# Optimization experiments

Hardware: AMD Instinct MI355X
Metric: run time of the kernel (lower is better)

Reference implementation:

```python
import jax, jax.numpy as jnp
import numpy as np

N_NODES = 100000
N_EDGES = 1600000
IN_CH = 128
OUT_CH = 128
EDGE_DIM = 6
STATE_DIM = 5


def setup_inputs() -> dict:
    key = jax.random.key(0)
    k = jax.random.split(key, 8)
    x = jax.random.normal(k[0], (N_NODES, IN_CH), dtype=jnp.float32)
    edge_index = jax.random.randint(k[1], (2, N_EDGES), 0, N_NODES, dtype=jnp.int64)
    edge_attr = jax.random.normal(k[2], (N_EDGES, EDGE_DIM), dtype=jnp.float32)
    global_state = jax.random.normal(k[3], (N_NODES, STATE_DIM), dtype=jnp.float32)
    # learned params (glorot init for weights, zero bias like torch default-ish)
    d_neg_in = IN_CH + EDGE_DIM + STATE_DIM
    d_root_in = IN_CH + STATE_DIM
    s_neg = jnp.sqrt(6.0 / (d_neg_in + OUT_CH))
    s_root = jnp.sqrt(6.0 / (d_root_in + OUT_CH))
    W_neg = jax.random.uniform(k[4], (d_neg_in, OUT_CH), jnp.float32, -s_neg, s_neg)
    b_neg = jax.random.uniform(k[5], (OUT_CH,), jnp.float32, -0.05, 0.05)
    W_root = jax.random.uniform(k[6], (d_root_in, OUT_CH), jnp.float32, -s_root, s_root)
    b_root = jax.random.uniform(k[7], (OUT_CH,), jnp.float32, -0.05, 0.05)
    return {"x": x, "edge_index": edge_index, "edge_attr": edge_attr,
            "global_state": global_state, "W_neg": W_neg, "b_neg": b_neg,
            "W_root": W_root, "b_root": b_root}


def reference(x, edge_index, edge_attr, global_state, W_neg, b_neg, W_root, b_root):
    # x: [N, C], global_state: [N, S]
    xs = jnp.concatenate([x, global_state], axis=1)            # [N, C+S]
    src = xs[edge_index[1]]                                    # gather: [E, C+S]
    x_adj = jnp.concatenate([src, edge_attr], axis=1)          # [E, C+S+Ed]
    x_adj = jax.nn.elu(x_adj @ W_neg + b_neg)                  # [E, O]
    neg_sum = jax.ops.segment_sum(x_adj, edge_index[0], num_segments=xs.shape[0])  # [N, O]
    x_out = jax.nn.elu(xs @ W_root + b_root) + neg_sum         # [N, O]
    return x_out
```

## Files before the change

kernel.cpp:

```cpp
#include <hip/hip_runtime.h>
#include <hip/hip_bf16.h>
#include <math.h>

#define N_NODES 100000
#define N_EDGES 1600000
#define IN_CH 128
#define OUT_CH 128
#define EDGE_DIM 6
#define STATE_DIM 5
#define XS_DIM 133
#define KPAD 160
#define NKSTEP 5
#define ASTRIDE 168
#define NBLK 391
#define N_CHUNKS 25000

typedef short s16x8 __attribute__((ext_vector_type(8)));
typedef float f32x4 __attribute__((ext_vector_type(4)));
typedef _Float16 h16x2 __attribute__((ext_vector_type(2)));

static __device__ __forceinline__ unsigned short f2bf(float f) {
    __hip_bfloat16 h = __float2bfloat16(f);
    return *reinterpret_cast<unsigned short*>(&h);
}
static __device__ __forceinline__ unsigned f2h(float f) {
    _Float16 h = (_Float16)f;
    return (unsigned)__builtin_bit_cast(unsigned short, h);
}
static __device__ __forceinline__ float bflo(unsigned u) {
    return __uint_as_float(u << 16);
}
static __device__ __forceinline__ float bfhi(unsigned u) {
    return __uint_as_float(u & 0xffff0000u);
}

static __device__ __forceinline__ float dot2f(unsigned a, h16x2 b, float c) {
#if __has_builtin(__builtin_amdgcn_fdot2)
    return __builtin_amdgcn_fdot2(__builtin_bit_cast(h16x2, a), b, c, false);
#else
    h16x2 av = __builtin_bit_cast(h16x2, a);
    return fmaf((float)av[0], (float)b[0], fmaf((float)av[1], (float)b[1], c));
#endif
}

__global__ __launch_bounds__(64) void repack_w(
    const float* __restrict__ Wneg, const float* __restrict__ Wroot,
    unsigned short* __restrict__ Pneg, unsigned short* __restrict__ Proot)
{
    int b = blockIdx.x;
    int mat = b / 40, r = b % 40;
    int kk = r / 8, nt = r % 8;
    int lane = threadIdx.x;
    const float* W = mat ? Wroot : Wneg;
    unsigned short* P = mat ? Proot : Pneg;
    int n = nt * 16 + (lane & 15);
    int kb = kk * 32 + (lane >> 4) * 8;
    unsigned short v[8];
#pragma unroll
    for (int j = 0; j < 8; ++j) {
        int k = kb + j;
        v[j] = (k < XS_DIM) ? f2bf(W[k * 128 + n]) : (unsigned short)0;
    }
    *(s16x8*)(P + ((size_t)(kk * 8 + nt) * 64 + lane) * 8) = *(s16x8*)v;
}

__global__ __launch_bounds__(256) void node_gemm_mfma(
    const float* __restrict__ x, const float* __restrict__ gs,
    const unsigned short* __restrict__ Pneg, const unsigned short* __restrict__ Proot,
    const float* __restrict__ bneg, const float* __restrict__ broot,
    __hip_bfloat16* __restrict__ Yb, float* __restrict__ out)
{
    __shared__ unsigned short Alds[64 * ASTRIDE];
    const int tid  = threadIdx.x;
    const int lane = tid & 63;
    const int wv   = tid >> 6;
    const int n0   = blockIdx.x * 64;

#pragma unroll
    for (int i = 0; i < 16; ++i) {
        int row = i * 4 + wv;
        int nn  = min(n0 + row, N_NODES - 1);
        const float2 v = *(const float2*)(x + (size_t)nn * IN_CH + lane * 2);
        Alds[row * ASTRIDE + lane * 2]     = f2bf(v.x);
        Alds[row * ASTRIDE + lane * 2 + 1] = f2bf(v.y);
    }
    if (tid < 64) {
        int nn = min(n0 + tid, N_NODES - 1);
#pragma unroll
        for (int j = 0; j < STATE_DIM; ++j)
            Alds[tid * ASTRIDE + IN_CH + j] = f2bf(gs[(size_t)nn * STATE_DIM + j]);
#pragma unroll
        for (int k = XS_DIM; k < KPAD; ++k)
            Alds[tid * ASTRIDE + k] = 0;
    }
    __syncthreads();

    f32x4 accN[8], accR[8];
    const f32x4 zero = {0.f, 0.f, 0.f, 0.f};
#pragma unroll
    for (int nt = 0; nt < 8; ++nt) { accN[nt] = zero; accR[nt] = zero; }

    const int m = lane & 15, quad = lane >> 4;
    const unsigned short* arow = Alds + (wv * 16 + m) * ASTRIDE + quad * 8;

    for (int kk = 0; kk < NKSTEP; ++kk) {
        s16x8 a = *(const s16x8*)(arow + kk * 32);
        const unsigned short* bp = Pneg  + ((size_t)kk * 8 * 64 + lane) * 8;
        const unsigned short* rp = Proot + ((size_t)kk * 8 * 64 + lane) * 8;
#pragma unroll
        for (int nt = 0; nt < 8; ++nt) {
            s16x8 bn = *(const s16x8*)(bp + nt * 512);
            accN[nt] = __builtin_amdgcn_mfma_f32_16x16x32_bf16(a, bn, accN[nt], 0, 0, 0);
            s16x8 br = *(const s16x8*)(rp + nt * 512);
            accR[nt] = __builtin_amdgcn_mfma_f32_16x16x32_bf16(a, br, accR[nt], 0, 0, 0);
        }
    }

#pragma unroll
    for (int nt = 0; nt < 8; ++nt) {
        int col = nt * 16 + m;
        float bn = bneg[col], br = broot[col];
        int rbase = n0 + wv * 16 + quad * 4;
#pragma unroll
        for (int r = 0; r < 4; ++r) {
            int node = rbase + r;
            if (node < N_NODES) {
                Yb[(size_t)node * 128 + col] = __float2bfloat16(accN[nt][r] + bn);
                float v = accR[nt][r] + br;
                out[(size_t)node * 128 + col] = (v > 0.f) ? v : (__expf(v) - 1.f);
            }
        }
    }
}

__global__ __launch_bounds__(256) void histogram(const int* __restrict__ idx,
                                                 int* __restrict__ cnt) {
    int e = blockIdx.x * 256 + threadIdx.x;
    if (e < N_EDGES) atomicAdd(&cnt[idx[e]], 1);
}

__global__ __launch_bounds__(256) void scan_block_sums(const int* __restrict__ cnt,
                                                       int* __restrict__ bsum) {
    __shared__ int ws[4];
    int tid = threadIdx.x, lane = tid & 63, wid = tid >> 6;
    int i = blockIdx.x * 256 + tid;
    int v = (i < N_NODES) ? cnt[i] : 0;
#pragma unroll
    for (int d = 32; d > 0; d >>= 1) v += __shfl_down(v, d);
    if (lane == 0) ws[wid] = v;
    __syncthreads();
    if (tid == 0) bsum[blockIdx.x] = ws[0] + ws[1] + ws[2] + ws[3];
}

__global__ __launch_bounds__(512) void scan_bsums(int* __restrict__ bsum) {
    __shared__ int s[512];
    int tid = threadIdx.x;
    int v = (tid < NBLK) ? bsum[tid] : 0;
    s[tid] = v;
    __syncthreads();
    for (int d = 1; d < 512; d <<= 1) {
        int t = (tid >= d) ? s[tid - d] : 0;
        __syncthreads();
        s[tid] += t;
        __syncthreads();
    }
    if (tid < NBLK) bsum[tid] = s[tid] - v;
}

__global__ __launch_bounds__(256) void scan_final(const int* __restrict__ cnt,
                                                  const int* __restrict__ bsum,
                                                  int* __restrict__ off,
                                                  int* __restrict__ cursor) {
    __shared__ int wsum[4];
    int tid = threadIdx.x, lane = tid & 63, wid = tid >> 6;
    int i = blockIdx.x * 256 + tid;
    int v = (i < N_NODES) ? cnt[i] : 0;
    int x = v;
#pragma unroll
    for (int d = 1; d < 64; d <<= 1) {
        int t = __shfl_up(x, d);
        if (lane >= d) x += t;
    }
    if (lane == 63) wsum[wid] = x;
    __syncthreads();
    int wpre = 0;
#pragma unroll
    for (int j = 0; j < 4; ++j) wpre += (j < wid) ? wsum[j] : 0;
    int excl = bsum[blockIdx.x] + wpre + x - v;
    if (i < N_NODES) { off[i] = excl; cursor[i] = excl; }
}

__global__ __launch_bounds__(256) void scatter_edges(const int* __restrict__ idx,
                                                     const float* __restrict__ ea,
                                                     int* __restrict__ cursor,
                                                     uint4* __restrict__ pay,
                                                     int* __restrict__ dstA) {
    int e = blockIdx.x * 256 + threadIdx.x;
    if (e < N_EDGES) {
        int dst = idx[e];
        int src = idx[N_EDGES + e];
        const float* er = ea + (size_t)e * EDGE_DIM;
        unsigned p0 = f2h(er[0]) | (f2h(er[1]) << 16);
        unsigned p1 = f2h(er[2]) | (f2h(er[3]) << 16);
        unsigned p2 = f2h(er[4]) | (f2h(er[5]) << 16);
        int pos = atomicAdd(&cursor[dst], 1);
        uint4 pl = { (unsigned)src, p0, p1, p2 };
        pay[pos] = pl;
        dstA[pos] = dst;
    }
}

__global__ __launch_bounds__(256) void aggregate(
    const uint4* __restrict__ pay,
    const int*  __restrict__ dstA,
    const float* __restrict__ Wneg,
    const __hip_bfloat16* __restrict__ Yb,
    float* __restrict__ out)
{
    const int lane = threadIdx.x & 63;
    const int wid  = blockIdx.x * 4 + (threadIdx.x >> 6);
    const int e0   = wid * 64;

    const float2* wb2 = (const float2*)(Wneg + 133 * 128);
    float2 w0 = wb2[0 * 64 + lane], w1 = wb2[1 * 64 + lane];
    float2 w2 = wb2[2 * 64 + lane], w3 = wb2[3 * 64 + lane];
    float2 w4 = wb2[4 * 64 + lane], w5 = wb2[5 * 64 + lane];
    h16x2 wx0 = {(_Float16)w0.x, (_Float16)w1.x};
    h16x2 wx1 = {(_Float16)w2.x, (_Float16)w3.x};
    h16x2 wx2 = {(_Float16)w4.x, (_Float16)w5.x};
    h16x2 wy0 = {(_Float16)w0.y, (_Float16)w1.y};
    h16x2 wy1 = {(_Float16)w2.y, (_Float16)w3.y};
    h16x2 wy2 = {(_Float16)w4.y, (_Float16)w5.y};

    const unsigned* Yu = (const unsigned*)Yb;

    uint4 pl = pay[e0 + lane];
    int src_l = (int)pl.x;
    int ea0 = (int)pl.y, ea1 = (int)pl.z, ea2 = (int)pl.w;
    int dst_l = dstA[e0 + lane];

    int nd = __shfl_down(dst_l, 1);
    unsigned long long bm = __ballot((lane == 63) || (dst_l != nd));

    float accx = 0.f, accy = 0.f;

    auto edge_op = [&](unsigned yv, int c) {
        unsigned a0 = (unsigned)__builtin_amdgcn_readlane(ea0, c);
        unsigned a1 = (unsigned)__builtin_amdgcn_readlane(ea1, c);
        unsigned a2 = (unsigned)__builtin_amdgcn_readlane(ea2, c);
        float tx = bflo(yv), ty = bfhi(yv);
        tx = dot2f(a0, wx0, tx); ty = dot2f(a0, wy0, ty);
        tx = dot2f(a1, wx1, tx); ty = dot2f(a1, wy1, ty);
        tx = dot2f(a2, wx2, tx); ty = dot2f(a2, wy2, ty);
        tx = (tx > 0.f) ? tx : (__expf(tx) - 1.f);
        ty = (ty > 0.f) ? ty : (__expf(ty) - 1.f);
        accx += tx; accy += ty;
        if ((bm >> c) & 1ull) {
            int n = __builtin_amdgcn_readlane(dst_l, c);
            float* orow = out + ((size_t)n << 7) + (lane << 1);
            atomicAdd(orow,     accx);
            atomicAdd(orow + 1, accy);
            accx = 0.f; accy = 0.f;
        }
    };

    auto load8 = [&](unsigned (&buf)[8], int pfbase) {
#pragma unroll
        for (int j = 0; j < 8; ++j) {
            int s = __builtin_amdgcn_readlane(src_l, pfbase + j);
            buf[j] = Yu[(size_t)s * 64 + lane];
        }
    };
    auto batch = [&](unsigned (&buf)[8], int cbase, int pfbase) {
#pragma unroll
        for (int j = 0; j < 8; ++j) {
            edge_op(buf[j], cbase + j);
            if (pfbase >= 0) {
                int s = __builtin_amdgcn_readlane(src_l, pfbase + j);
                buf[j] = Yu[(size_t)s * 64 + lane];
            }
        }
    };

    unsigned yA[8], yB[8], yC[8];
    load8(yA, 0); load8(yB, 8); load8(yC, 16);

    batch(yA,  0, 24);
    batch(yB,  8, 32);
    batch(yC, 16, 40);
    batch(yA, 24, 48);
    batch(yB, 32, 56);
    batch(yC, 40, -1);
    batch(yA, 48, -1);
    batch(yB, 56, -1);
}

extern "C" void kernel_launch(void* const* d_in, const int* in_sizes, int n_in,
                              void* d_out, int out_size, void* d_ws, size_t ws_size,
                              hipStream_t stream) {
    const float* x     = (const float*)d_in[0];
    const int*   idx   = (const int*)  d_in[1];
    const float* ea    = (const float*)d_in[2];
    const float* gs    = (const float*)d_in[3];
    const float* Wneg  = (const float*)d_in[4];
    const float* bneg  = (const float*)d_in[5];
    const float* Wroot = (const float*)d_in[6];
    const float* broot = (const float*)d_in[7];
    float* out = (float*)d_out;

    char* w = (char*)d_ws;
    __hip_bfloat16* Yb = (__hip_bfloat16*)w;      w += (size_t)N_NODES * 128 * 2;
    int* cnt  = (int*)w;                          w += (size_t)N_NODES * 4;
    int* off  = (int*)w;                          w += (size_t)N_NODES * 4;
    int* cur  = (int*)w;                          w += (size_t)N_NODES * 4;
    int* bsum = (int*)w;                          w += 2048;
    uint4* pay = (uint4*)w;                       w += (size_t)N_EDGES * 16;
    int* dstA = (int*)w;                          w += (size_t)N_EDGES * 4;
    unsigned short* Pneg  = (unsigned short*)w;   w += (size_t)NKSTEP * 8 * 64 * 8 * 2;
    unsigned short* Proot = (unsigned short*)w;

    const int nb_edges = (N_EDGES + 255) / 256;

    repack_w<<<80, 64, 0, stream>>>(Wneg, Wroot, Pneg, Proot);
    node_gemm_mfma<<<(N_NODES + 63) / 64, 256, 0, stream>>>(
        x, gs, Pneg, Proot, bneg, broot, Yb, out);
    hipMemsetAsync(cnt, 0, (size_t)N_NODES * 4, stream);
    histogram<<<nb_edges, 256, 0, stream>>>(idx, cnt);
    scan_block_sums<<<NBLK, 256, 0, stream>>>(cnt, bsum);
    scan_bsums<<<1, 512, 0, stream>>>(bsum);
    scan_final<<<NBLK, 256, 0, stream>>>(cnt, bsum, off, cur);
    scatter_edges<<<nb_edges, 256, 0, stream>>>(idx, ea, cur, pay, dstA);
    aggregate<<<N_CHUNKS / 4, 256, 0, stream>>>(pay, dstA, Wneg, Yb, out);
}
```

Baseline: 460.1 us.

## Fill sorted dst array in scan and defer segment atomics via LDS staging

The destination array is now written in sorted order by the scan kernel instead of by scattered writes in scatter_edges, which turns random stores into contiguous ones. In the aggregate kernel the first MAXSEG per-segment partial sums are staged in shared memory and flushed with atomics after all edge computation, so the atomic traffic no longer sits inside the gather and compute loop. Each scan thread now loops over its own node's edges with per-thread serial stores, and the extra LDS use may lower occupancy.

```diff
diff --git a/kernel.cpp b/kernel.cpp
--- a/kernel.cpp
+++ b/kernel.cpp
@@ -14,6 +14,7 @@
 #define ASTRIDE 168
 #define NBLK 391
 #define N_CHUNKS 25000
+#define MAXSEG 8
 
 typedef short s16x8 __attribute__((ext_vector_type(8)));
 typedef float f32x4 __attribute__((ext_vector_type(4)));
@@ -170,7 +171,8 @@
 __global__ __launch_bounds__(256) void scan_final(const int* __restrict__ cnt,
                                                   const int* __restrict__ bsum,
                                                   int* __restrict__ off,
-                                                  int* __restrict__ cursor) {
+                                                  int* __restrict__ cursor,
+                                                  int* __restrict__ dstA) {
     __shared__ int wsum[4];
     int tid = threadIdx.x, lane = tid & 63, wid = tid >> 6;
     int i = blockIdx.x * 256 + tid;
@@ -187,14 +189,16 @@
 #pragma unroll
     for (int j = 0; j < 4; ++j) wpre += (j < wid) ? wsum[j] : 0;
     int excl = bsum[blockIdx.x] + wpre + x - v;
-    if (i < N_NODES) { off[i] = excl; cursor[i] = excl; }
+    if (i < N_NODES) {
+        off[i] = excl; cursor[i] = excl;
+        for (int j = 0; j < v; ++j) dstA[excl + j] = i;
+    }
 }
 
 __global__ __launch_bounds__(256) void scatter_edges(const int* __restrict__ idx,
                                                      const float* __restrict__ ea,
                                                      int* __restrict__ cursor,
-                                                     uint4* __restrict__ pay,
-                                                     int* __restrict__ dstA) {
+                                                     uint4* __restrict__ pay) {
     int e = blockIdx.x * 256 + threadIdx.x;
     if (e < N_EDGES) {
         int dst = idx[e];
@@ -206,7 +210,6 @@
         int pos = atomicAdd(&cursor[dst], 1);
         uint4 pl = { (unsigned)src, p0, p1, p2 };
         pay[pos] = pl;
-        dstA[pos] = dst;
     }
 }
 
@@ -217,8 +220,11 @@
     const __hip_bfloat16* __restrict__ Yb,
     float* __restrict__ out)
 {
+    __shared__ float2 fl[4][MAXSEG][64];
+
     const int lane = threadIdx.x & 63;
-    const int wid  = blockIdx.x * 4 + (threadIdx.x >> 6);
+    const int wv   = threadIdx.x >> 6;
+    const int wid  = blockIdx.x * 4 + wv;
     const int e0   = wid * 64;
 
     const float2* wb2 = (const float2*)(Wneg + 133 * 128);
@@ -243,6 +249,7 @@
     unsigned long long bm = __ballot((lane == 63) || (dst_l != nd));
 
     float accx = 0.f, accy = 0.f;
+    int seg = 0;
 
     auto edge_op = [&](unsigned yv, int c) {
         unsigned a0 = (unsigned)__builtin_amdgcn_readlane(ea0, c);
@@ -256,10 +263,15 @@
         ty = (ty > 0.f) ? ty : (__expf(ty) - 1.f);
         accx += tx; accy += ty;
         if ((bm >> c) & 1ull) {
-            int n = __builtin_amdgcn_readlane(dst_l, c);
-            float* orow = out + ((size_t)n << 7) + (lane << 1);
-            atomicAdd(orow,     accx);
-            atomicAdd(orow + 1, accy);
+            if (seg < MAXSEG) {
+                fl[wv][seg][lane] = make_float2(accx, accy);
+            } else {
+                int n = __builtin_amdgcn_readlane(dst_l, c);
+                float* orow = out + ((size_t)n << 7) + (lane << 1);
+                atomicAdd(orow,     accx);
+                atomicAdd(orow + 1, accy);
+            }
+            ++seg;
             accx = 0.f; accy = 0.f;
         }
     };
@@ -293,6 +305,19 @@
     batch(yC, 40, -1);
     batch(yA, 48, -1);
     batch(yB, 56, -1);
+
+    unsigned long long rem = bm;
+#pragma unroll
+    for (int s = 0; s < MAXSEG; ++s) {
+        if (rem == 0ull) break;
+        int pos = __builtin_ctzll(rem);
+        rem &= rem - 1ull;
+        int n = __builtin_amdgcn_readlane(dst_l, pos);
+        float2 v = fl[wv][s][lane];
+        float* orow = out + ((size_t)n << 7) + (lane << 1);
+        atomicAdd(orow,     v.x);
+        atomicAdd(orow + 1, v.y);
+    }
 }
 
 extern "C" void kernel_launch(void* const* d_in, const int* in_sizes, int n_in,
@@ -328,7 +353,7 @@
     histogram<<<nb_edges, 256, 0, stream>>>(idx, cnt);
     scan_block_sums<<<NBLK, 256, 0, stream>>>(cnt, bsum);
     scan_bsums<<<1, 512, 0, stream>>>(bsum);
-    scan_final<<<NBLK, 256, 0, stream>>>(cnt, bsum, off, cur);
-    scatter_edges<<<nb_edges, 256, 0, stream>>>(idx, ea, cur, pay, dstA);
+    scan_final<<<NBLK, 256, 0, stream>>>(cnt, bsum, off, cur, dstA);
+    scatter_edges<<<nb_edges, 256, 0, stream>>>(idx, ea, cur, pay);
     aggregate<<<N_CHUNKS / 4, 256, 0, stream>>>(pay, dstA, Wneg, Yb, out);
 }
```

Result: slower. 475.9 us (+3.4%).

## Fuse CSR build into one cooperative kernel with grid syncs

Applied to the files above, without the earlier changes.

Replaces the memset, histogram, three scan kernels and scatter kernel with a single cooperative kernel that uses grid-wide syncs between phases. dstA is now filled per node from the scan instead of being written by each edge in the scatter. Nontemporal loads and stores are added on streaming data, and the node GEMM's LDS fill is packed into 32-bit writes. This is meant to cut launch overhead and scattered stores, at the cost of grid-sync latency and fixed occupancy from 1024 blocks.

```diff
diff --git a/kernel.cpp b/kernel.cpp
--- a/kernel.cpp
+++ b/kernel.cpp
@@ -1,6 +1,9 @@
 #include <hip/hip_runtime.h>
 #include <hip/hip_bf16.h>
+#include <hip/hip_cooperative_groups.h>
 #include <math.h>
+
+namespace cg = cooperative_groups;
 
 #define N_NODES 100000
 #define N_EDGES 1600000
@@ -14,9 +17,12 @@
 #define ASTRIDE 168
 #define NBLK 391
 #define N_CHUNKS 25000
+#define CSR_BLOCKS 1024
 
 typedef short s16x8 __attribute__((ext_vector_type(8)));
 typedef float f32x4 __attribute__((ext_vector_type(4)));
+typedef float f32x2 __attribute__((ext_vector_type(2)));
+typedef unsigned u32x4 __attribute__((ext_vector_type(4)));
 typedef _Float16 h16x2 __attribute__((ext_vector_type(2)));
 
 static __device__ __forceinline__ unsigned short f2bf(float f) {
@@ -80,18 +86,21 @@
     for (int i = 0; i < 16; ++i) {
         int row = i * 4 + wv;
         int nn  = min(n0 + row, N_NODES - 1);
-        const float2 v = *(const float2*)(x + (size_t)nn * IN_CH + lane * 2);
-        Alds[row * ASTRIDE + lane * 2]     = f2bf(v.x);
-        Alds[row * ASTRIDE + lane * 2 + 1] = f2bf(v.y);
-    }
-    if (tid < 64) {
-        int nn = min(n0 + tid, N_NODES - 1);
-#pragma unroll
-        for (int j = 0; j < STATE_DIM; ++j)
-            Alds[tid * ASTRIDE + IN_CH + j] = f2bf(gs[(size_t)nn * STATE_DIM + j]);
-#pragma unroll
-        for (int k = XS_DIM; k < KPAD; ++k)
-            Alds[tid * ASTRIDE + k] = 0;
+        const f32x2 v = __builtin_nontemporal_load(
+            (const f32x2*)(x + (size_t)nn * IN_CH) + lane);
+        unsigned pk = (unsigned)f2bf(v.x) | ((unsigned)f2bf(v.y) << 16);
+        *(unsigned*)(&Alds[row * ASTRIDE + lane * 2]) = pk;
+    }
+#pragma unroll
+    for (int s2 = 0; s2 < 4; ++s2) {
+        int slot = tid * 4 + s2;
+        int row  = slot >> 4;
+        int cp   = slot & 15;
+        int nn   = min(n0 + row, N_NODES - 1);
+        int c0   = IN_CH + cp * 2;
+        unsigned lo = (c0     < XS_DIM) ? (unsigned)f2bf(gs[(size_t)nn * STATE_DIM + (c0 - IN_CH)])     : 0u;
+        unsigned hi = (c0 + 1 < XS_DIM) ? (unsigned)f2bf(gs[(size_t)nn * STATE_DIM + (c0 + 1 - IN_CH)]) : 0u;
+        *(unsigned*)(&Alds[row * ASTRIDE + c0]) = lo | (hi << 16);
     }
     __syncthreads();
 
@@ -133,80 +142,100 @@
     }
 }
 
-__global__ __launch_bounds__(256) void histogram(const int* __restrict__ idx,
-                                                 int* __restrict__ cnt) {
-    int e = blockIdx.x * 256 + threadIdx.x;
-    if (e < N_EDGES) atomicAdd(&cnt[idx[e]], 1);
-}
-
-__global__ __launch_bounds__(256) void scan_block_sums(const int* __restrict__ cnt,
-                                                       int* __restrict__ bsum) {
-    __shared__ int ws[4];
-    int tid = threadIdx.x, lane = tid & 63, wid = tid >> 6;
-    int i = blockIdx.x * 256 + tid;
-    int v = (i < N_NODES) ? cnt[i] : 0;
-#pragma unroll
-    for (int d = 32; d > 0; d >>= 1) v += __shfl_down(v, d);
-    if (lane == 0) ws[wid] = v;
-    __syncthreads();
-    if (tid == 0) bsum[blockIdx.x] = ws[0] + ws[1] + ws[2] + ws[3];
-}
-
-__global__ __launch_bounds__(512) void scan_bsums(int* __restrict__ bsum) {
-    __shared__ int s[512];
-    int tid = threadIdx.x;
-    int v = (tid < NBLK) ? bsum[tid] : 0;
-    s[tid] = v;
-    __syncthreads();
-    for (int d = 1; d < 512; d <<= 1) {
-        int t = (tid >= d) ? s[tid - d] : 0;
+__global__ __launch_bounds__(256) void build_csr(
+    const int* __restrict__ idx, const float* __restrict__ ea,
+    int* __restrict__ cnt, int* __restrict__ bsum,
+    int* __restrict__ off, int* __restrict__ cur,
+    int* __restrict__ dstA, uint4* __restrict__ pay)
+{
+    cg::grid_group grid = cg::this_grid();
+    __shared__ int shm[8];
+
+    const int tid   = threadIdx.x;
+    const int bid   = blockIdx.x;
+    const int lane  = tid & 63;
+    const int wv    = tid >> 6;
+    const int gsize = CSR_BLOCKS * 256;
+    const int gtid  = bid * 256 + tid;
+
+    for (int i = gtid; i < N_NODES; i += gsize) cnt[i] = 0;
+    grid.sync();
+
+    for (int e = gtid; e < N_EDGES; e += gsize) {
+        int d = __builtin_nontemporal_load(idx + e);
+        atomicAdd(&cnt[d], 1);
+    }
+    grid.sync();
+
+    if (bid < NBLK) {
+        int i = bid * 256 + tid;
+        int v = (i < N_NODES) ? cnt[i] : 0;
+#pragma unroll
+        for (int d = 32; d > 0; d >>= 1) v += __shfl_down(v, d);
+        if (lane == 0) shm[wv] = v;
         __syncthreads();
-        s[tid] += t;
+        if (tid == 0) bsum[bid] = shm[0] + shm[1] + shm[2] + shm[3];
+    }
+    grid.sync();
+
+    if (bid == 0) {
+        int e0 = tid * 2, e1 = tid * 2 + 1;
+        int v0 = (e0 < NBLK) ? bsum[e0] : 0;
+        int v1 = (e1 < NBLK) ? bsum[e1] : 0;
+        int p = v0 + v1;
+        int xx = p;
+#pragma unroll
+        for (int d = 1; d < 64; d <<= 1) {
+            int t = __shfl_up(xx, d);
+            if (lane >= d) xx += t;
+        }
+        if (lane == 63) shm[wv] = xx;
         __syncthreads();
-    }
-    if (tid < NBLK) bsum[tid] = s[tid] - v;
-}
-
-__global__ __launch_bounds__(256) void scan_final(const int* __restrict__ cnt,
-                                                  const int* __restrict__ bsum,
-                                                  int* __restrict__ off,
-                                                  int* __restrict__ cursor) {
-    __shared__ int wsum[4];
-    int tid = threadIdx.x, lane = tid & 63, wid = tid >> 6;
-    int i = blockIdx.x * 256 + tid;
-    int v = (i < N_NODES) ? cnt[i] : 0;
-    int x = v;
-#pragma unroll
-    for (int d = 1; d < 64; d <<= 1) {
-        int t = __shfl_up(x, d);
-        if (lane >= d) x += t;
-    }
-    if (lane == 63) wsum[wid] = x;
-    __syncthreads();
-    int wpre = 0;
-#pragma unroll
-    for (int j = 0; j < 4; ++j) wpre += (j < wid) ? wsum[j] : 0;
-    int excl = bsum[blockIdx.x] + wpre + x - v;
-    if (i < N_NODES) { off[i] = excl; cursor[i] = excl; }
-}
-
-__global__ __launch_bounds__(256) void scatter_edges(const int* __restrict__ idx,
-                                                     const float* __restrict__ ea,
-                                                     int* __restrict__ cursor,
-                                                     uint4* __restrict__ pay,
-                                                     int* __restrict__ dstA) {
-    int e = blockIdx.x * 256 + threadIdx.x;
-    if (e < N_EDGES) {
-        int dst = idx[e];
-        int src = idx[N_EDGES + e];
-        const float* er = ea + (size_t)e * EDGE_DIM;
-        unsigned p0 = f2h(er[0]) | (f2h(er[1]) << 16);
-        unsigned p1 = f2h(er[2]) | (f2h(er[3]) << 16);
-        unsigned p2 = f2h(er[4]) | (f2h(er[5]) << 16);
-        int pos = atomicAdd(&cursor[dst], 1);
-        uint4 pl = { (unsigned)src, p0, p1, p2 };
-        pay[pos] = pl;
-        dstA[pos] = dst;
+        int wpre = 0;
+#pragma unroll
+        for (int j = 0; j < 4; ++j) wpre += (j < wv) ? shm[j] : 0;
+        int excl_pair = wpre + xx - p;
+        if (e0 < NBLK) bsum[e0] = excl_pair;
+        if (e1 < NBLK) bsum[e1] = excl_pair + v0;
+    }
+    grid.sync();
+
+    if (bid < NBLK) {
+        int i = bid * 256 + tid;
+        int v = (i < N_NODES) ? cnt[i] : 0;
+        int xx = v;
+#pragma unroll
+        for (int d = 1; d < 64; d <<= 1) {
+            int t = __shfl_up(xx, d);
+            if (lane >= d) xx += t;
+        }
+        __syncthreads();
+        if (lane == 63) shm[wv] = xx;
+        __syncthreads();
+        int wpre = 0;
+#pragma unroll
+        for (int j = 0; j < 4; ++j) wpre += (j < wv) ? shm[j] : 0;
+        int excl = bsum[bid] + wpre + xx - v;
+        if (i < N_NODES) {
+            off[i] = excl; cur[i] = excl;
+            for (int j = 0; j < v; ++j) dstA[excl + j] = i;
+        }
+    }
+    grid.sync();
+
+    for (int e = gtid; e < N_EDGES; e += gsize) {
+        int dst = __builtin_nontemporal_load(idx + e);
+        int src = __builtin_nontemporal_load(idx + N_EDGES + e);
+        const f32x2* er = (const f32x2*)(ea + (size_t)e * EDGE_DIM);
+        f32x2 e01 = __builtin_nontemporal_load(er);
+        f32x2 e23 = __builtin_nontemporal_load(er + 1);
+        f32x2 e45 = __builtin_nontemporal_load(er + 2);
+        unsigned p0 = f2h(e01.x) | (f2h(e01.y) << 16);
+        unsigned p1 = f2h(e23.x) | (f2h(e23.y) << 16);
+        unsigned p2 = f2h(e45.x) | (f2h(e45.y) << 16);
+        int pos = atomicAdd(&cur[dst], 1);
+        u32x4 pl = { (unsigned)src, p0, p1, p2 };
+        __builtin_nontemporal_store(pl, (u32x4*)pay + pos);
     }
 }
 
@@ -221,10 +250,10 @@
     const int wid  = blockIdx.x * 4 + (threadIdx.x >> 6);
     const int e0   = wid * 64;
 
-    const float2* wb2 = (const float2*)(Wneg + 133 * 128);
-    float2 w0 = wb2[0 * 64 + lane], w1 = wb2[1 * 64 + lane];
-    float2 w2 = wb2[2 * 64 + lane], w3 = wb2[3 * 64 + lane];
-    float2 w4 = wb2[4 * 64 + lane], w5 = wb2[5 * 64 + lane];
+    const f32x2* wb2 = (const f32x2*)(Wneg + 133 * 128);
+    f32x2 w0 = wb2[0 * 64 + lane], w1 = wb2[1 * 64 + lane];
+    f32x2 w2 = wb2[2 * 64 + lane], w3 = wb2[3 * 64 + lane];
+    f32x2 w4 = wb2[4 * 64 + lane], w5 = wb2[5 * 64 + lane];
     h16x2 wx0 = {(_Float16)w0.x, (_Float16)w1.x};
     h16x2 wx1 = {(_Float16)w2.x, (_Float16)w3.x};
     h16x2 wx2 = {(_Float16)w4.x, (_Float16)w5.x};
@@ -234,10 +263,10 @@
 
     const unsigned* Yu = (const unsigned*)Yb;
 
-    uint4 pl = pay[e0 + lane];
+    u32x4 pl = __builtin_nontemporal_load((const u32x4*)pay + e0 + lane);
     int src_l = (int)pl.x;
     int ea0 = (int)pl.y, ea1 = (int)pl.z, ea2 = (int)pl.w;
-    int dst_l = dstA[e0 + lane];
+    int dst_l = __builtin_nontemporal_load(dstA + e0 + lane);
 
     int nd = __shfl_down(dst_l, 1);
     unsigned long long bm = __ballot((lane == 63) || (dst_l != nd));
@@ -319,16 +348,16 @@
     unsigned short* Pneg  = (unsigned short*)w;   w += (size_t)NKSTEP * 8 * 64 * 8 * 2;
     unsigned short* Proot = (unsigned short*)w;
 
-    const int nb_edges = (N_EDGES + 255) / 256;
-
     repack_w<<<80, 64, 0, stream>>>(Wneg, Wroot, Pneg, Proot);
     node_gemm_mfma<<<(N_NODES + 63) / 64, 256, 0, stream>>>(
         x, gs, Pneg, Proot, bneg, broot, Yb, out);
-    hipMemsetAsync(cnt, 0, (size_t)N_NODES * 4, stream);
-    histogram<<<nb_edges, 256, 0, stream>>>(idx, cnt);
-    scan_block_sums<<<NBLK, 256, 0, stream>>>(cnt, bsum);
-    scan_bsums<<<1, 512, 0, stream>>>(bsum);
-    scan_final<<<NBLK, 256, 0, stream>>>(cnt, bsum, off, cur);
-    scatter_edges<<<nb_edges, 256, 0, stream>>>(idx, ea, cur, pay, dstA);
+
+    {
+        void* args[] = { (void*)&idx, (void*)&ea, (void*)&cnt, (void*)&bsum,
+                         (void*)&off, (void*)&cur, (void*)&dstA, (void*)&pay };
+        (void)hipLaunchCooperativeKernel((const void*)build_csr,
+                                         dim3(CSR_BLOCKS), dim3(256), args, 0, stream);
+    }
+
     aggregate<<<N_CHUNKS / 4, 256, 0, stream>>>(pay, dstA, Wneg, Yb, out);
 }
```

New measurement: 952.8 us. 2.07x slower.
